# Optimization experiments

Hardware: AMD Instinct MI355X
Metric: run time of the kernel (lower is better)

Reference implementation:

```python
import jax, jax.numpy as jnp
import numpy as np

N = 4096          # n_nodes
D = 7             # ligand_dim
H = 8             # dim_h
CUTOFF = 3.6      # bond_cutoff


def _linear_init(key, fan_in, fan_out):
    k1, k2 = jax.random.split(key)
    s = 1.0 / np.sqrt(fan_in)
    w = jax.random.uniform(k1, (fan_in, fan_out), minval=-s, maxval=s, dtype=jnp.float32)
    b = jax.random.uniform(k2, (fan_out,), minval=-s, maxval=s, dtype=jnp.float32)
    return w, b


def setup_inputs() -> dict:
    key = jax.random.key(0)
    ks = jax.random.split(key, 6)
    w1, b1 = _linear_init(ks[0], D, H)          # model layer 1
    w2, b2 = _linear_init(ks[1], H, H)          # model layer 2
    w3, b3 = _linear_init(ks[2], H, D + 16)     # model layer 3 (feats | keys | queries)
    we, be = _linear_init(ks[3], 2 * D, H)      # encoder
    wd, bd = _linear_init(ks[4], H, D)          # decoder
    x = jax.random.normal(ks[5], (N, D), dtype=jnp.float32)
    return dict(x=x, w1=w1, b1=b1, w2=w2, b2=b2, w3=w3, b3=b3,
                we=we, be=be, wd=wd, bd=bd)


def reference(x, w1, b1, w2, b2, w3, b3, we, be, wd, bd):
    # --- build_graph on detached x: L1 distance over first 3 coords ---
    # (sum(sqrt(abs(a-b)**2)) == sum(abs(a-b)))
    pos = jax.lax.stop_gradient(x[:, :3])
    dist = jnp.zeros((N, N), dtype=x.dtype)
    for d in range(3):  # loop over 3 coords to avoid an [N,N,3] intermediate
        dist = dist + jnp.abs(pos[:, d][:, None] - pos[None, :, d])
    A = (dist <= CUTOFF).astype(x.dtype)  # [N, N] adjacency
    # temp_input[-1] is never reset in the original kk loop, so node kk's
    # attention list is the cumulative multiset of neighbors of nodes 0..kk.
    C = jnp.cumsum(A, axis=0)             # [N, N] multiplicity of node l in kk's list

    # --- tiny MLP (shared per node) ---
    h = jnp.arctan(x @ w1 + b1)
    h = jnp.arctan(h @ w2 + b2)
    m = h @ w3 + b3                       # [N, D+16]
    feats = m[:, :D]                      # aggregated message payload
    keys_ = m[:, D:D + 8]                 # temp[:, -16:-8]
    queries = m[:, D + 8:]                # temp[:, -8:]

    # attention score of a list element depends only on its source node:
    # score = dot(queries[mm], keys[mm])
    s = jnp.sum(queries * keys_, axis=1)  # [N]

    # softmax over the cumulative multiset: weight of node l in row kk is
    # C[kk,l] * exp(s_l) / sum_l' C[kk,l'] * exp(s_l')   (stable via masked max)
    mask = C > 0
    smax = jnp.max(jnp.where(mask, s[None, :], -jnp.inf), axis=1)    # [N]
    w = C * jnp.where(mask, jnp.exp(s[None, :] - smax[:, None]), 0.0)  # [N, N]
    agg = (w @ feats) / jnp.sum(w, axis=1, keepdims=True)            # [N, D]

    # --- encode / decode ---
    codes = jnp.arctan(jnp.concatenate([x, agg], axis=1) @ we + be)  # [N, H]
    new_graph = codes @ wd + bd                                      # [N, D]
    return new_graph
```

## Files before the change

kernel.cpp:

```cpp
#include <hip/hip_runtime.h>
#include <math.h>

#define NN 4096
#define DD 7
#define HH 8
#define CUT 3.6f
#define JSPLIT 4
#define JCH (NN / JSPLIT)
#define RB 32


__global__ __launch_bounds__(256) void k_mlp(
    const float* __restrict__ x,
    const float* __restrict__ w1, const float* __restrict__ b1,
    const float* __restrict__ w2, const float* __restrict__ b2,
    const float* __restrict__ w3, const float* __restrict__ b3,
    float* __restrict__ node, float* __restrict__ bmax)
{
    int t = threadIdx.x;
    int n = blockIdx.x * 256 + t;
    float xi[DD];
#pragma unroll
    for (int i = 0; i < DD; ++i) xi[i] = x[n * DD + i];

    float h1[HH];
#pragma unroll
    for (int o = 0; o < HH; ++o) {
        float a = b1[o];
#pragma unroll
        for (int i = 0; i < DD; ++i) a = fmaf(xi[i], w1[i * HH + o], a);
        h1[o] = atanf(a);
    }
    float h2[HH];
#pragma unroll
    for (int o = 0; o < HH; ++o) {
        float a = b2[o];
#pragma unroll
        for (int i = 0; i < HH; ++i) a = fmaf(h1[i], w2[i * HH + o], a);
        h2[o] = atanf(a);
    }
    float m[23];
#pragma unroll
    for (int c = 0; c < 23; ++c) {
        float a = b3[c];
#pragma unroll
        for (int i = 0; i < HH; ++i) a = fmaf(h2[i], w3[i * 23 + c], a);
        m[c] = a;
    }
    float s = 0.f;
#pragma unroll
    for (int k = 0; k < 8; ++k) s = fmaf(m[15 + k], m[7 + k], s);

    float4* nd4 = (float4*)(node + n * 12);
    nd4[0] = make_float4(xi[0], xi[1], xi[2], s);
    nd4[1] = make_float4(m[0], m[1], m[2], m[3]);
    nd4[2] = make_float4(m[4], m[5], m[6], 0.f);

    float v = s;
#pragma unroll
    for (int off = 32; off > 0; off >>= 1) v = fmaxf(v, __shfl_xor(v, off, 64));
    __shared__ float wm[4];
    if ((t & 63) == 0) wm[t >> 6] = v;
    __syncthreads();
    if (t == 0)
        bmax[blockIdx.x] = fmaxf(fmaxf(wm[0], wm[1]), fmaxf(wm[2], wm[3]));
}

__global__ __launch_bounds__(256) void k_pair(const float* __restrict__ node,
                                              const float* __restrict__ bmax,
                                              float* __restrict__ part)
{
    __shared__ float4 tile[JCH * 3];
    int xb = blockIdx.x;
    int y  = blockIdx.y;
    int t  = threadIdx.x;

    float gm = bmax[0];
#pragma unroll
    for (int i = 1; i < 16; ++i) gm = fmaxf(gm, bmax[i]);

    const float4* node4 = (const float4*)node;
    int base = y * JCH * 3;
#pragma unroll
    for (int q = 0; q < 4; ++q) {
        int j = q * 256 + t;
        float4 a = node4[base + j * 3 + 0];
        float4 b = node4[base + j * 3 + 1];
        float4 c = node4[base + j * 3 + 2];
        float e = expf(a.w - gm);
        tile[j * 3 + 0] = make_float4(a.x, a.y, a.z, e);
        tile[j * 3 + 1] = make_float4(e * b.x, e * b.y, e * b.z, e * b.w);
        tile[j * 3 + 2] = make_float4(e * c.x, e * c.y, e * c.z, 0.f);
    }
    __syncthreads();

    int jl = t & 31;
    int rg = t >> 5;
    int r0 = xb * RB + rg * 4;

    float p[4][3];
#pragma unroll
    for (int rr = 0; rr < 4; ++rr) {
        const float* nd = node + (r0 + rr) * 12;
        p[rr][0] = nd[0]; p[rr][1] = nd[1]; p[rr][2] = nd[2];
    }
    float acc[4][8];
#pragma unroll
    for (int rr = 0; rr < 4; ++rr)
#pragma unroll
        for (int ch = 0; ch < 8; ++ch) acc[rr][ch] = 0.f;

    for (int jj = jl; jj < JCH; jj += 32) {
        float4 a = tile[jj * 3 + 0];
        float4 b = tile[jj * 3 + 1];
        float4 c = tile[jj * 3 + 2];
#pragma unroll
        for (int rr = 0; rr < 4; ++rr) {
            float dist = fabsf(p[rr][0] - a.x) + fabsf(p[rr][1] - a.y)
                       + fabsf(p[rr][2] - a.z);
            float msel = (dist <= CUT) ? 1.0f : 0.0f;
            acc[rr][0] = fmaf(msel, b.x, acc[rr][0]);
            acc[rr][1] = fmaf(msel, b.y, acc[rr][1]);
            acc[rr][2] = fmaf(msel, b.z, acc[rr][2]);
            acc[rr][3] = fmaf(msel, b.w, acc[rr][3]);
            acc[rr][4] = fmaf(msel, c.x, acc[rr][4]);
            acc[rr][5] = fmaf(msel, c.y, acc[rr][5]);
            acc[rr][6] = fmaf(msel, c.z, acc[rr][6]);
            acc[rr][7] = fmaf(msel, a.w, acc[rr][7]);
        }
    }

#pragma unroll
    for (int rr = 0; rr < 4; ++rr)
#pragma unroll
        for (int ch = 0; ch < 8; ++ch) {
            float v = acc[rr][ch];
            v += __shfl_xor(v, 16, 32);
            v += __shfl_xor(v, 8, 32);
            v += __shfl_xor(v, 4, 32);
            v += __shfl_xor(v, 2, 32);
            v += __shfl_xor(v, 1, 32);
            acc[rr][ch] = v;
        }

    if (jl == 0) {
#pragma unroll
        for (int rr = 0; rr < 4; ++rr) {
#pragma unroll
            for (int ch = 0; ch < 8; ++ch)
                part[(size_t)(y * 8 + ch) * NN + (r0 + rr)] = acc[rr][ch];
        }
    }
}

__global__ __launch_bounds__(256) void k_scan(const float* __restrict__ part,
                                              float* __restrict__ prefix)
{
    int c = blockIdx.x;
    int t = threadIdx.x;

    const float4* p0 = (const float4*)(part + (size_t)(0 * 8 + c) * NN);
    const float4* p1 = (const float4*)(part + (size_t)(1 * 8 + c) * NN);
    const float4* p2 = (const float4*)(part + (size_t)(2 * 8 + c) * NN);
    const float4* p3 = (const float4*)(part + (size_t)(3 * 8 + c) * NN);

    float vals[16];
#pragma unroll
    for (int q = 0; q < 4; ++q) {
        int i4 = t * 4 + q;
        float4 a = p0[i4], b = p1[i4], cc = p2[i4], d = p3[i4];
        vals[q * 4 + 0] = (a.x + b.x) + (cc.x + d.x);
        vals[q * 4 + 1] = (a.y + b.y) + (cc.y + d.y);
        vals[q * 4 + 2] = (a.z + b.z) + (cc.z + d.z);
        vals[q * 4 + 3] = (a.w + b.w) + (cc.w + d.w);
    }
    float ts = 0.f;
#pragma unroll
    for (int e = 0; e < 16; ++e) ts += vals[e];

    int lane = t & 63, wv = t >> 6;
    float v = ts;
#pragma unroll
    for (int off = 1; off < 64; off <<= 1) {
        float o = __shfl_up(v, off, 64);
        if (lane >= off) v += o;
    }
    __shared__ float wtot[4];
    if (lane == 63) wtot[wv] = v;
    __syncthreads();
    float woff = 0.f;
    for (int w = 0; w < 4; ++w) if (w < wv) woff += wtot[w];
    float run = woff + v - ts;

    float pr[16];
#pragma unroll
    for (int e = 0; e < 16; ++e) { run += vals[e]; pr[e] = run; }
    float4* out4 = (float4*)(prefix + (size_t)c * NN + t * 16);
#pragma unroll
    for (int q = 0; q < 4; ++q)
        out4[q] = make_float4(pr[q * 4 + 0], pr[q * 4 + 1], pr[q * 4 + 2], pr[q * 4 + 3]);
}

__global__ __launch_bounds__(256) void k_final(
    const float* __restrict__ x, const float* __restrict__ prefix,
    const float* __restrict__ we, const float* __restrict__ be,
    const float* __restrict__ wd, const float* __restrict__ bd,
    float* __restrict__ out)
{
    int n = blockIdx.x * 256 + threadIdx.x;
    float v[14];
#pragma unroll
    for (int i = 0; i < DD; ++i) v[i] = x[n * DD + i];
    float den = prefix[(size_t)7 * NN + n];
#pragma unroll
    for (int d = 0; d < DD; ++d) v[DD + d] = prefix[(size_t)d * NN + n] / den;

    float codes[HH];
#pragma unroll
    for (int o = 0; o < HH; ++o) {
        float a = be[o];
#pragma unroll
        for (int i = 0; i < 14; ++i) a = fmaf(v[i], we[i * HH + o], a);
        codes[o] = atanf(a);
    }
#pragma unroll
    for (int d = 0; d < DD; ++d) {
        float a = bd[d];
#pragma unroll
        for (int o = 0; o < HH; ++o) a = fmaf(codes[o], wd[o * DD + d], a);
        out[n * DD + d] = a;
    }
}

extern "C" void kernel_launch(void* const* d_in, const int* in_sizes, int n_in,
                              void* d_out, int out_size, void* d_ws, size_t ws_size,
                              hipStream_t stream)
{
    const float* x  = (const float*)d_in[0];
    const float* w1 = (const float*)d_in[1];
    const float* b1 = (const float*)d_in[2];
    const float* w2 = (const float*)d_in[3];
    const float* b2 = (const float*)d_in[4];
    const float* w3 = (const float*)d_in[5];
    const float* b3 = (const float*)d_in[6];
    const float* we = (const float*)d_in[7];
    const float* be = (const float*)d_in[8];
    const float* wd = (const float*)d_in[9];
    const float* bd = (const float*)d_in[10];
    float* out = (float*)d_out;

    float* ws     = (float*)d_ws;
    float* node   = ws;
    float* part   = node + NN * 12;
    float* prefix = part + 4 * 8 * NN;
    float* bmax   = prefix + 8 * NN;

    k_mlp  <<<NN / 256, 256, 0, stream>>>(x, w1, b1, w2, b2, w3, b3, node, bmax);
    k_pair <<<dim3(NN / RB, JSPLIT), 256, 0, stream>>>(node, bmax, part);
    k_scan <<<8, 256, 0, stream>>>(part, prefix);
    k_final<<<NN / 256, 256, 0, stream>>>(x, prefix, we, be, wd, bd, out);
}
```

Baseline: 29.49 us.

## Fuse MLP into pair kernel, drop max-shift, merge scan with final stage

Reduces four kernels to two. The per-node MLP is recomputed inside each pair block for its 256-node column chunk, and the global max shift for the softmax is removed, so plain exp(s) is used. The pair kernel now gives each thread one row with no cross-lane reductions, over a 16x16 grid. The scan is fused into the final encode/decode kernel, where each block recomputes its own base offset by summing all earlier partials. This removes launches and intermediate buffers, but it also cuts the pair grid to 256 blocks, makes the MLP work redundant across blocks, and risks exp overflow without the max shift.

```diff
diff --git a/kernel.cpp b/kernel.cpp
--- a/kernel.cpp
+++ b/kernel.cpp
@@ -5,215 +5,165 @@
 #define DD 7
 #define HH 8
 #define CUT 3.6f
-#define JSPLIT 4
-#define JCH (NN / JSPLIT)
-#define RB 32
-
-
-__global__ __launch_bounds__(256) void k_mlp(
+#define TPB 256
+#define JSPLIT 16
+#define JCH 256
+#define NRT 16
+
+
+__global__ __launch_bounds__(TPB) void k_pair(
     const float* __restrict__ x,
     const float* __restrict__ w1, const float* __restrict__ b1,
     const float* __restrict__ w2, const float* __restrict__ b2,
     const float* __restrict__ w3, const float* __restrict__ b3,
-    float* __restrict__ node, float* __restrict__ bmax)
-{
-    int t = threadIdx.x;
-    int n = blockIdx.x * 256 + t;
-    float xi[DD];
-#pragma unroll
-    for (int i = 0; i < DD; ++i) xi[i] = x[n * DD + i];
-
-    float h1[HH];
-#pragma unroll
-    for (int o = 0; o < HH; ++o) {
-        float a = b1[o];
-#pragma unroll
-        for (int i = 0; i < DD; ++i) a = fmaf(xi[i], w1[i * HH + o], a);
-        h1[o] = atanf(a);
-    }
-    float h2[HH];
-#pragma unroll
-    for (int o = 0; o < HH; ++o) {
-        float a = b2[o];
-#pragma unroll
-        for (int i = 0; i < HH; ++i) a = fmaf(h1[i], w2[i * HH + o], a);
-        h2[o] = atanf(a);
-    }
-    float m[23];
-#pragma unroll
-    for (int c = 0; c < 23; ++c) {
-        float a = b3[c];
-#pragma unroll
-        for (int i = 0; i < HH; ++i) a = fmaf(h2[i], w3[i * 23 + c], a);
-        m[c] = a;
-    }
-    float s = 0.f;
-#pragma unroll
-    for (int k = 0; k < 8; ++k) s = fmaf(m[15 + k], m[7 + k], s);
-
-    float4* nd4 = (float4*)(node + n * 12);
-    nd4[0] = make_float4(xi[0], xi[1], xi[2], s);
-    nd4[1] = make_float4(m[0], m[1], m[2], m[3]);
-    nd4[2] = make_float4(m[4], m[5], m[6], 0.f);
-
-    float v = s;
-#pragma unroll
-    for (int off = 32; off > 0; off >>= 1) v = fmaxf(v, __shfl_xor(v, off, 64));
-    __shared__ float wm[4];
-    if ((t & 63) == 0) wm[t >> 6] = v;
-    __syncthreads();
-    if (t == 0)
-        bmax[blockIdx.x] = fmaxf(fmaxf(wm[0], wm[1]), fmaxf(wm[2], wm[3]));
-}
-
-__global__ __launch_bounds__(256) void k_pair(const float* __restrict__ node,
-                                              const float* __restrict__ bmax,
-                                              float* __restrict__ part)
+    float* __restrict__ part)
 {
     __shared__ float4 tile[JCH * 3];
-    int xb = blockIdx.x;
-    int y  = blockIdx.y;
-    int t  = threadIdx.x;
-
-    float gm = bmax[0];
-#pragma unroll
-    for (int i = 1; i < 16; ++i) gm = fmaxf(gm, bmax[i]);
-
-    const float4* node4 = (const float4*)node;
-    int base = y * JCH * 3;
-#pragma unroll
-    for (int q = 0; q < 4; ++q) {
-        int j = q * 256 + t;
-        float4 a = node4[base + j * 3 + 0];
-        float4 b = node4[base + j * 3 + 1];
-        float4 c = node4[base + j * 3 + 2];
-        float e = expf(a.w - gm);
-        tile[j * 3 + 0] = make_float4(a.x, a.y, a.z, e);
-        tile[j * 3 + 1] = make_float4(e * b.x, e * b.y, e * b.z, e * b.w);
-        tile[j * 3 + 2] = make_float4(e * c.x, e * c.y, e * c.z, 0.f);
+    const int xb = blockIdx.x;
+    const int y  = blockIdx.y;
+    const int t  = threadIdx.x;
+
+    {
+        const int jg = y * JCH + t;
+        float xi[DD];
+#pragma unroll
+        for (int i = 0; i < DD; ++i) xi[i] = x[jg * DD + i];
+
+        float h1[HH];
+#pragma unroll
+        for (int o = 0; o < HH; ++o) {
+            float a = b1[o];
+#pragma unroll
+            for (int i = 0; i < DD; ++i) a = fmaf(xi[i], w1[i * HH + o], a);
+            h1[o] = atanf(a);
+        }
+        float h2[HH];
+#pragma unroll
+        for (int o = 0; o < HH; ++o) {
+            float a = b2[o];
+#pragma unroll
+            for (int i = 0; i < HH; ++i) a = fmaf(h1[i], w2[i * HH + o], a);
+            h2[o] = atanf(a);
+        }
+        float m[23];
+#pragma unroll
+        for (int c = 0; c < 23; ++c) {
+            float a = b3[c];
+#pragma unroll
+            for (int i = 0; i < HH; ++i) a = fmaf(h2[i], w3[i * 23 + c], a);
+            m[c] = a;
+        }
+        float s = 0.f;
+#pragma unroll
+        for (int k = 0; k < 8; ++k) s = fmaf(m[15 + k], m[7 + k], s);
+        const float e = expf(s);
+
+        tile[t * 3 + 0] = make_float4(xi[0], xi[1], xi[2], e);
+        tile[t * 3 + 1] = make_float4(e * m[0], e * m[1], e * m[2], e * m[3]);
+        tile[t * 3 + 2] = make_float4(e * m[4], e * m[5], e * m[6], 0.f);
     }
     __syncthreads();
 
-    int jl = t & 31;
-    int rg = t >> 5;
-    int r0 = xb * RB + rg * 4;
-
-    float p[4][3];
-#pragma unroll
-    for (int rr = 0; rr < 4; ++rr) {
-        const float* nd = node + (r0 + rr) * 12;
-        p[rr][0] = nd[0]; p[rr][1] = nd[1]; p[rr][2] = nd[2];
-    }
-    float acc[4][8];
-#pragma unroll
-    for (int rr = 0; rr < 4; ++rr)
-#pragma unroll
-        for (int ch = 0; ch < 8; ++ch) acc[rr][ch] = 0.f;
-
-    for (int jj = jl; jj < JCH; jj += 32) {
-        float4 a = tile[jj * 3 + 0];
-        float4 b = tile[jj * 3 + 1];
-        float4 c = tile[jj * 3 + 2];
-#pragma unroll
-        for (int rr = 0; rr < 4; ++rr) {
-            float dist = fabsf(p[rr][0] - a.x) + fabsf(p[rr][1] - a.y)
-                       + fabsf(p[rr][2] - a.z);
-            float msel = (dist <= CUT) ? 1.0f : 0.0f;
-            acc[rr][0] = fmaf(msel, b.x, acc[rr][0]);
-            acc[rr][1] = fmaf(msel, b.y, acc[rr][1]);
-            acc[rr][2] = fmaf(msel, b.z, acc[rr][2]);
-            acc[rr][3] = fmaf(msel, b.w, acc[rr][3]);
-            acc[rr][4] = fmaf(msel, c.x, acc[rr][4]);
-            acc[rr][5] = fmaf(msel, c.y, acc[rr][5]);
-            acc[rr][6] = fmaf(msel, c.z, acc[rr][6]);
-            acc[rr][7] = fmaf(msel, a.w, acc[rr][7]);
-        }
-    }
-
-#pragma unroll
-    for (int rr = 0; rr < 4; ++rr)
-#pragma unroll
-        for (int ch = 0; ch < 8; ++ch) {
-            float v = acc[rr][ch];
-            v += __shfl_xor(v, 16, 32);
-            v += __shfl_xor(v, 8, 32);
-            v += __shfl_xor(v, 4, 32);
-            v += __shfl_xor(v, 2, 32);
-            v += __shfl_xor(v, 1, 32);
-            acc[rr][ch] = v;
-        }
-
-    if (jl == 0) {
-#pragma unroll
-        for (int rr = 0; rr < 4; ++rr) {
-#pragma unroll
-            for (int ch = 0; ch < 8; ++ch)
-                part[(size_t)(y * 8 + ch) * NN + (r0 + rr)] = acc[rr][ch];
-        }
-    }
+    const int row = xb * TPB + t;
+    const float p0 = x[row * DD + 0];
+    const float p1 = x[row * DD + 1];
+    const float p2 = x[row * DD + 2];
+
+    float acc[8];
+#pragma unroll
+    for (int ch = 0; ch < 8; ++ch) acc[ch] = 0.f;
+
+#pragma unroll 4
+    for (int j = 0; j < JCH; ++j) {
+        float4 a = tile[j * 3 + 0];
+        float4 b = tile[j * 3 + 1];
+        float4 c = tile[j * 3 + 2];
+        float dist = fabsf(p0 - a.x) + fabsf(p1 - a.y) + fabsf(p2 - a.z);
+        float msel = (dist <= CUT) ? 1.0f : 0.0f;
+        acc[0] = fmaf(msel, b.x, acc[0]);
+        acc[1] = fmaf(msel, b.y, acc[1]);
+        acc[2] = fmaf(msel, b.z, acc[2]);
+        acc[3] = fmaf(msel, b.w, acc[3]);
+        acc[4] = fmaf(msel, c.x, acc[4]);
+        acc[5] = fmaf(msel, c.y, acc[5]);
+        acc[6] = fmaf(msel, c.z, acc[6]);
+        acc[7] = fmaf(msel, a.w, acc[7]);
+    }
+#pragma unroll
+    for (int ch = 0; ch < 8; ++ch)
+        part[(size_t)(y * 8 + ch) * NN + row] = acc[ch];
 }
 
-__global__ __launch_bounds__(256) void k_scan(const float* __restrict__ part,
-                                              float* __restrict__ prefix)
-{
-    int c = blockIdx.x;
-    int t = threadIdx.x;
-
-    const float4* p0 = (const float4*)(part + (size_t)(0 * 8 + c) * NN);
-    const float4* p1 = (const float4*)(part + (size_t)(1 * 8 + c) * NN);
-    const float4* p2 = (const float4*)(part + (size_t)(2 * 8 + c) * NN);
-    const float4* p3 = (const float4*)(part + (size_t)(3 * 8 + c) * NN);
-
-    float vals[16];
-#pragma unroll
-    for (int q = 0; q < 4; ++q) {
-        int i4 = t * 4 + q;
-        float4 a = p0[i4], b = p1[i4], cc = p2[i4], d = p3[i4];
-        vals[q * 4 + 0] = (a.x + b.x) + (cc.x + d.x);
-        vals[q * 4 + 1] = (a.y + b.y) + (cc.y + d.y);
-        vals[q * 4 + 2] = (a.z + b.z) + (cc.z + d.z);
-        vals[q * 4 + 3] = (a.w + b.w) + (cc.w + d.w);
-    }
-    float ts = 0.f;
-#pragma unroll
-    for (int e = 0; e < 16; ++e) ts += vals[e];
-
-    int lane = t & 63, wv = t >> 6;
-    float v = ts;
-#pragma unroll
-    for (int off = 1; off < 64; off <<= 1) {
-        float o = __shfl_up(v, off, 64);
-        if (lane >= off) v += o;
-    }
-    __shared__ float wtot[4];
-    if (lane == 63) wtot[wv] = v;
-    __syncthreads();
-    float woff = 0.f;
-    for (int w = 0; w < 4; ++w) if (w < wv) woff += wtot[w];
-    float run = woff + v - ts;
-
-    float pr[16];
-#pragma unroll
-    for (int e = 0; e < 16; ++e) { run += vals[e]; pr[e] = run; }
-    float4* out4 = (float4*)(prefix + (size_t)c * NN + t * 16);
-#pragma unroll
-    for (int q = 0; q < 4; ++q)
-        out4[q] = make_float4(pr[q * 4 + 0], pr[q * 4 + 1], pr[q * 4 + 2], pr[q * 4 + 3]);
-}
-
-__global__ __launch_bounds__(256) void k_final(
-    const float* __restrict__ x, const float* __restrict__ prefix,
+__global__ __launch_bounds__(TPB) void k_scanfinal(
+    const float* __restrict__ x, const float* __restrict__ part,
     const float* __restrict__ we, const float* __restrict__ be,
     const float* __restrict__ wd, const float* __restrict__ bd,
     float* __restrict__ out)
 {
-    int n = blockIdx.x * 256 + threadIdx.x;
+    const int b = blockIdx.x;
+    const int t = threadIdx.x;
+
+    __shared__ float sbase[8];
+    __shared__ float wtot[4][8];
+
+    {
+        const int ch = t >> 5, lane = t & 31;
+        float bs = 0.f;
+        const int n4 = b * 64;
+        for (int k4 = lane; k4 < n4; k4 += 32) {
+#pragma unroll
+            for (int y = 0; y < JSPLIT; ++y) {
+                const float4* p4 = (const float4*)(part + (size_t)(y * 8 + ch) * NN);
+                float4 v = p4[k4];
+                bs += (v.x + v.y) + (v.z + v.w);
+            }
+        }
+#pragma unroll
+        for (int off = 16; off > 0; off >>= 1) bs += __shfl_xor(bs, off, 32);
+        if (lane == 0) sbase[ch] = bs;
+    }
+
+    const int k = b * TPB + t;
+    float T[8];
+#pragma unroll
+    for (int ch = 0; ch < 8; ++ch) {
+        float v = 0.f;
+#pragma unroll
+        for (int y = 0; y < JSPLIT; ++y)
+            v += part[(size_t)(y * 8 + ch) * NN + k];
+        T[ch] = v;
+    }
+
+    const int lane = t & 63, wv = t >> 6;
+    float sc[8];
+#pragma unroll
+    for (int ch = 0; ch < 8; ++ch) {
+        float v = T[ch];
+#pragma unroll
+        for (int off = 1; off < 64; off <<= 1) {
+            float o = __shfl_up(v, off, 64);
+            if (lane >= off) v += o;
+        }
+        if (lane == 63) wtot[wv][ch] = v;
+        sc[ch] = v;
+    }
+    __syncthreads();
+
+    float pref[8];
+#pragma unroll
+    for (int ch = 0; ch < 8; ++ch) {
+        float woff = sbase[ch];
+#pragma unroll
+        for (int w = 0; w < 4; ++w) if (w < wv) woff += wtot[w][ch];
+        pref[ch] = woff + sc[ch];
+    }
+
     float v[14];
 #pragma unroll
-    for (int i = 0; i < DD; ++i) v[i] = x[n * DD + i];
-    float den = prefix[(size_t)7 * NN + n];
-#pragma unroll
-    for (int d = 0; d < DD; ++d) v[DD + d] = prefix[(size_t)d * NN + n] / den;
+    for (int i = 0; i < DD; ++i) v[i] = x[k * DD + i];
+    const float den = pref[7];
+#pragma unroll
+    for (int d = 0; d < DD; ++d) v[DD + d] = pref[d] / den;
 
     float codes[HH];
 #pragma unroll
@@ -228,7 +178,7 @@
         float a = bd[d];
 #pragma unroll
         for (int o = 0; o < HH; ++o) a = fmaf(codes[o], wd[o * DD + d], a);
-        out[n * DD + d] = a;
+        out[k * DD + d] = a;
     }
 }
 
@@ -249,14 +199,8 @@
     const float* bd = (const float*)d_in[10];
     float* out = (float*)d_out;
 
-    float* ws     = (float*)d_ws;
-    float* node   = ws;
-    float* part   = node + NN * 12;
-    float* prefix = part + 4 * 8 * NN;
-    float* bmax   = prefix + 8 * NN;
-
-    k_mlp  <<<NN / 256, 256, 0, stream>>>(x, w1, b1, w2, b2, w3, b3, node, bmax);
-    k_pair <<<dim3(NN / RB, JSPLIT), 256, 0, stream>>>(node, bmax, part);
-    k_scan <<<8, 256, 0, stream>>>(part, prefix);
-    k_final<<<NN / 256, 256, 0, stream>>>(x, prefix, we, be, wd, bd, out);
+    float* part = (float*)d_ws;
+
+    k_pair     <<<dim3(NRT, JSPLIT), TPB, 0, stream>>>(x, w1, b1, w2, b2, w3, b3, part);
+    k_scanfinal<<<NRT, TPB, 0, stream>>>(x, part, we, be, wd, bd, out);
 }
```

Measured after the change: 44.77 us. 51.8% more time.
